# Performance work log

Hardware: AMD Instinct MI355X
Metric: run time of the kernel (lower is better)

Reference implementation:

```python
import jax, jax.numpy as jnp
from jax import lax
import numpy as np

RADIUS = 0.2
NSAMPLE = 64


def _ball_query(xyz, new_xyz, radius, nsample):
    """Faithful PointNet++ ball query.

    For each center, take the first `nsample` point indices (in index order)
    whose squared distance < radius^2; if fewer than nsample are found, the
    remaining slots are filled with the first found index (CUDA kernel
    semantics). Returns int32 idx of shape (B, npoint, nsample).
    """
    N = xyz.shape[1]
    # (B, npoint, N) squared distances
    d2 = jnp.sum((new_xyz[:, :, None, :] - xyz[:, None, :, :]) ** 2, axis=-1)
    within = d2 < (radius * radius)
    # key = point index if within ball, else N (sentinel); smallest nsample
    # keys == first nsample in-ball indices in index order.
    key = jnp.where(within, jnp.arange(N, dtype=jnp.int32), jnp.int32(N))
    neg_vals, _ = lax.top_k(-key, nsample)          # largest of -key = smallest key
    sel = -neg_vals                                  # (B, npoint, nsample)
    valid = sel < N
    first = jnp.where(valid[..., :1], sel[..., :1], 0)  # first found idx (or 0)
    return jnp.where(valid, sel, first)


def _group_gather(features, idx):
    # features: (B, C, N), idx: (B, npoint, nsample) -> (B, C, npoint, nsample)
    return jax.vmap(lambda f, i: f[:, i])(features, idx)


def setup_inputs() -> dict:
    key = jax.random.key(0)
    k1, k2, k3 = jax.random.split(key, 3)
    B, N, npoint, C = 4, 16384, 2048, 64
    xyz = jax.random.uniform(k1, (B, N, 3), dtype=jnp.float32)
    new_xyz = jax.random.uniform(k2, (B, npoint, 3), dtype=jnp.float32)
    features = jax.random.normal(k3, (B, C, N), dtype=jnp.float32)
    return {"xyz": xyz, "new_xyz": new_xyz, "features": features}


def reference(xyz, new_xyz, features):
    idx = _ball_query(xyz, new_xyz, RADIUS, NSAMPLE)          # (B, npoint, nsample)
    xyz_t = jnp.transpose(xyz, (0, 2, 1))                      # (B, 3, N)
    grouped_xyz = _group_gather(xyz_t, idx)                    # (B, 3, npoint, nsample)
    grouped_xyz = grouped_xyz - jnp.transpose(new_xyz, (0, 2, 1))[..., None]
    grouped_features = _group_gather(features, idx)            # (B, C, npoint, nsample)
    new_features = jnp.concatenate([grouped_xyz, grouped_features], axis=1)
    # original code does .transpose(1, 2) -> (B, npoint, 3+C, nsample)
    return jnp.transpose(new_features, (0, 2, 1, 3))
```

## Files before the change

### kernel.cpp

```cpp
#include <hip/hip_runtime.h>


#define BB 4
#define NN 16384
#define NP 2048
#define CC 64
#define NS 64
#define CH (3 + CC)
#define NCHUNK (NN / 256)

__global__ __launch_bounds__(256) void pn2_prep_kernel(
    const float* __restrict__ xyz,
    const float* __restrict__ new_xyz,
    const float* __restrict__ features,
    float* __restrict__ ft,
    int* __restrict__ idxbuf,
    float* __restrict__ out)
{
    __shared__ float tile[CC][65];
    __shared__ int sidx[4][NS];

    if (blockIdx.x < BB * 256) {
        const int b   = blockIdx.x >> 8;
        const int n0  = (blockIdx.x & 255) << 6;
        const int col = threadIdx.x & 63;
        const int r4  = threadIdx.x >> 6;
        const float* src = features + (size_t)b * CC * NN;
#pragma unroll
        for (int i = 0; i < 16; ++i) {
            const int c = r4 + i * 4;
            tile[c][col] = src[(size_t)c * NN + n0 + col];
        }
        __syncthreads();
        float* dst = ft + ((size_t)b * NN + n0) * CC;
#pragma unroll
        for (int i = 0; i < 16; ++i) {
            const int n = r4 + i * 4;
            dst[(size_t)n * CC + col] = tile[col][n];
        }
        return;
    }

    const int lane = threadIdx.x & 63;
    const int wave = threadIdx.x >> 6;
    const int center = (blockIdx.x - BB * 256) * 4 + wave;
    const int b = center >> 11;
    const int j = center & (NP - 1);

    const float r2 = 0.04f;
    const float* q = new_xyz + ((size_t)b * NP + j) * 3;
    const float cx = q[0], cy = q[1], cz = q[2];

    const float* xb = xyz + (size_t)b * NN * 3;
    const float4* x4 = (const float4*)xb;
    int* widx = sidx[wave];

    const int base = 3 * lane;
    int found = 0;
    int it = 0;
    float4 A = x4[base], Bv = x4[base + 1], Cv = x4[base + 2];

    while (true) {
        const int nit = (it + 1 < NCHUNK) ? it + 1 : it;
        const size_t nb = (size_t)nit * 192 + base;
        float4 nA = x4[nb], nB = x4[nb + 1], nC = x4[nb + 2];

        const int n0 = it * 256 + 4 * lane;
        const float px[4] = {A.x, A.w, Bv.z, Cv.y};
        const float py[4] = {A.y, Bv.x, Bv.w, Cv.z};
        const float pz[4] = {A.z, Bv.y, Cv.x, Cv.w};
        bool in[4];
        unsigned long long m[4];
#pragma unroll
        for (int k = 0; k < 4; ++k) {
            const float dx = px[k] - cx;
            const float dy = py[k] - cy;
            const float dz = pz[k] - cz;
            const float d2 = __fadd_rn(__fadd_rn(__fmul_rn(dx, dx), __fmul_rn(dy, dy)),
                                       __fmul_rn(dz, dz));
            in[k] = d2 < r2;
            m[k] = __ballot(in[k]);
        }
        const unsigned long long low = (1ull << lane) - 1ull;
        int pos = found
                + (int)__popcll(m[0] & low) + (int)__popcll(m[1] & low)
                + (int)__popcll(m[2] & low) + (int)__popcll(m[3] & low);
#pragma unroll
        for (int k = 0; k < 4; ++k) {
            if (in[k]) {
                if (pos < NS) widx[pos] = n0 + k;
                ++pos;
            }
        }
        found += (int)(__popcll(m[0]) + __popcll(m[1])
                     + __popcll(m[2]) + __popcll(m[3]));
        if (found >= NS || it == NCHUNK - 1) break;
        A = nA; Bv = nB; Cv = nC; ++it;
    }

    int myidx = 0;
    if (found > 0) {
        const int first = widx[0];
        myidx = (lane < found) ? widx[lane] : first;
    }
    idxbuf[(size_t)center * NS + lane] = myidx;

    const float* pp = xb + (size_t)myidx * 3;
    float* ob = out + ((size_t)center * CH) * NS + lane;
    __builtin_nontemporal_store(pp[0] - cx, ob + 0 * NS);
    __builtin_nontemporal_store(pp[1] - cy, ob + 1 * NS);
    __builtin_nontemporal_store(pp[2] - cz, ob + 2 * NS);
}

__global__ __launch_bounds__(256) void pn2_gather_kernel(
    const float* __restrict__ ft,
    const int* __restrict__ idxbuf,
    float* __restrict__ out)
{
    const int center = blockIdx.x;
    const int b = center >> 11;
    const int lane = threadIdx.x & 63;
    const int w = threadIdx.x >> 6;

    const int myidx = idxbuf[(size_t)center * NS + lane];
    const float4* row = (const float4*)(ft + ((size_t)b * NN + myidx) * CC) + 4 * w;
    const float4 v0 = row[0], v1 = row[1], v2 = row[2], v3 = row[3];

    float* ob = out + ((size_t)center * CH + 3 + 16 * w) * NS + lane;
    __builtin_nontemporal_store(v0.x, ob + 0 * NS);
    __builtin_nontemporal_store(v0.y, ob + 1 * NS);
    __builtin_nontemporal_store(v0.z, ob + 2 * NS);
    __builtin_nontemporal_store(v0.w, ob + 3 * NS);
    __builtin_nontemporal_store(v1.x, ob + 4 * NS);
    __builtin_nontemporal_store(v1.y, ob + 5 * NS);
    __builtin_nontemporal_store(v1.z, ob + 6 * NS);
    __builtin_nontemporal_store(v1.w, ob + 7 * NS);
    __builtin_nontemporal_store(v2.x, ob + 8 * NS);
    __builtin_nontemporal_store(v2.y, ob + 9 * NS);
    __builtin_nontemporal_store(v2.z, ob + 10 * NS);
    __builtin_nontemporal_store(v2.w, ob + 11 * NS);
    __builtin_nontemporal_store(v3.x, ob + 12 * NS);
    __builtin_nontemporal_store(v3.y, ob + 13 * NS);
    __builtin_nontemporal_store(v3.z, ob + 14 * NS);
    __builtin_nontemporal_store(v3.w, ob + 15 * NS);
}

__global__ __launch_bounds__(256, 4) void pn2_group_kernel(
    const float* __restrict__ xyz, const float* __restrict__ new_xyz,
    const float* __restrict__ features, float* __restrict__ out)
{
    __shared__ int sidx[4][NS];
    const int lane = threadIdx.x & 63;
    const int wave = threadIdx.x >> 6;
    const int center = blockIdx.x * 4 + wave;
    const int b = center >> 11;
    const int j = center & (NP - 1);
    const float r2 = 0.04f;
    const float* q = new_xyz + ((size_t)b * NP + j) * 3;
    const float cx = q[0], cy = q[1], cz = q[2];
    int* widx = sidx[wave];
    int found = 0;
    for (int it = 0; it < NN / 64; ++it) {
        const int n = it * 64 + lane;
        const float* p = xyz + ((size_t)b * NN + n) * 3;
        const float dx = p[0] - cx, dy = p[1] - cy, dz = p[2] - cz;
        const float d2 = __fadd_rn(__fadd_rn(__fmul_rn(dx, dx), __fmul_rn(dy, dy)),
                                   __fmul_rn(dz, dz));
        const bool within = d2 < r2;
        const unsigned long long mask = __ballot(within);
        const int pos = found + (int)__popcll(mask & ((1ull << lane) - 1ull));
        if (within && pos < NS) widx[pos] = n;
        found += (int)__popcll(mask);
        if (found >= NS) break;
    }
    int myidx = 0;
    if (found > 0) {
        const int first = widx[0];
        myidx = (lane < found) ? widx[lane] : first;
    }
    const float* pp = xyz + ((size_t)b * NN + myidx) * 3;
    float* ob = out + (((size_t)b * NP + j) * (size_t)CH) * NS + lane;
    ob[0 * NS] = pp[0] - cx;
    ob[1 * NS] = pp[1] - cy;
    ob[2 * NS] = pp[2] - cz;
    const float* fb = features + (size_t)b * CC * NN + myidx;
#pragma unroll 8
    for (int c = 0; c < CC; ++c) ob[(size_t)(3 + c) * NS] = fb[(size_t)c * NN];
}

extern "C" void kernel_launch(void* const* d_in, const int* in_sizes, int n_in,
                              void* d_out, int out_size, void* d_ws, size_t ws_size,
                              hipStream_t stream) {
    const float* xyz      = (const float*)d_in[0];
    const float* new_xyz  = (const float*)d_in[1];
    const float* features = (const float*)d_in[2];
    float* out = (float*)d_out;

    const size_t ft_bytes  = (size_t)BB * NN * CC * sizeof(float);
    const size_t idx_bytes = (size_t)BB * NP * NS * sizeof(int);

    if (ws_size >= ft_bytes + idx_bytes) {
        float* ft   = (float*)d_ws;
        int* idxbuf = (int*)((char*)d_ws + ft_bytes);
        pn2_prep_kernel<<<BB * 256 + BB * NP / 4, 256, 0, stream>>>(
            xyz, new_xyz, features, ft, idxbuf, out);
        pn2_gather_kernel<<<BB * NP, 256, 0, stream>>>(ft, idxbuf, out);
    } else {
        pn2_group_kernel<<<BB * NP / 4, 256, 0, stream>>>(xyz, new_xyz, features, out);
    }
}
```

Before: 54.52 us.

## Fuse ball query with feature gather, split transpose into its own kernel

The feature transpose moves into a separate kernel, and the ball query is fused with the feature gather, so each wave writes its center's whole output row directly. This drops the idx buffer round trip through global memory and one launch, but makes the transpose and query serial rather than co-scheduled in one grid. Each lane now loads a full 256-byte feature row (16 float4s in two batches of 8), which raises register pressure per wave. The transpose also switches to nontemporal loads.

```diff
diff --git a/kernel.cpp b/kernel.cpp
--- a/kernel.cpp
+++ b/kernel.cpp
@@ -9,41 +9,40 @@
 #define CH (3 + CC)
 #define NCHUNK (NN / 256)
 
-__global__ __launch_bounds__(256) void pn2_prep_kernel(
+__global__ __launch_bounds__(256) void pn2_transpose_kernel(
+    const float* __restrict__ f, float* __restrict__ ft)
+{
+    __shared__ float tile[CC][65];
+    const int b   = blockIdx.x >> 8;
+    const int n0  = (blockIdx.x & 255) << 6;
+    const int col = threadIdx.x & 63;
+    const int r4  = threadIdx.x >> 6;
+    const float* src = f + (size_t)b * CC * NN;
+#pragma unroll
+    for (int i = 0; i < 16; ++i) {
+        const int c = r4 + i * 4;
+        tile[c][col] = __builtin_nontemporal_load(&src[(size_t)c * NN + n0 + col]);
+    }
+    __syncthreads();
+    float* dst = ft + ((size_t)b * NN + n0) * CC;
+#pragma unroll
+    for (int i = 0; i < 16; ++i) {
+        const int n = r4 + i * 4;
+        dst[(size_t)n * CC + col] = tile[col][n];
+    }
+}
+
+__global__ __launch_bounds__(256, 4) void pn2_qg_kernel(
     const float* __restrict__ xyz,
     const float* __restrict__ new_xyz,
-    const float* __restrict__ features,
-    float* __restrict__ ft,
-    int* __restrict__ idxbuf,
+    const float* __restrict__ ft,
     float* __restrict__ out)
 {
-    __shared__ float tile[CC][65];
     __shared__ int sidx[4][NS];
-
-    if (blockIdx.x < BB * 256) {
-        const int b   = blockIdx.x >> 8;
-        const int n0  = (blockIdx.x & 255) << 6;
-        const int col = threadIdx.x & 63;
-        const int r4  = threadIdx.x >> 6;
-        const float* src = features + (size_t)b * CC * NN;
-#pragma unroll
-        for (int i = 0; i < 16; ++i) {
-            const int c = r4 + i * 4;
-            tile[c][col] = src[(size_t)c * NN + n0 + col];
-        }
-        __syncthreads();
-        float* dst = ft + ((size_t)b * NN + n0) * CC;
-#pragma unroll
-        for (int i = 0; i < 16; ++i) {
-            const int n = r4 + i * 4;
-            dst[(size_t)n * CC + col] = tile[col][n];
-        }
-        return;
-    }
 
     const int lane = threadIdx.x & 63;
     const int wave = threadIdx.x >> 6;
-    const int center = (blockIdx.x - BB * 256) * 4 + wave;
+    const int center = blockIdx.x * 4 + wave;
     const int b = center >> 11;
     const int j = center & (NP - 1);
 
@@ -56,6 +55,7 @@
     int* widx = sidx[wave];
 
     const int base = 3 * lane;
+    const unsigned long long low = (1ull << lane) - 1ull;
     int found = 0;
     int it = 0;
     float4 A = x4[base], Bv = x4[base + 1], Cv = x4[base + 2];
@@ -81,7 +81,6 @@
             in[k] = d2 < r2;
             m[k] = __ballot(in[k]);
         }
-        const unsigned long long low = (1ull << lane) - 1ull;
         int pos = found
                 + (int)__popcll(m[0] & low) + (int)__popcll(m[1] & low)
                 + (int)__popcll(m[2] & low) + (int)__popcll(m[3] & low);
@@ -103,46 +102,28 @@
         const int first = widx[0];
         myidx = (lane < found) ? widx[lane] : first;
     }
-    idxbuf[(size_t)center * NS + lane] = myidx;
 
     const float* pp = xb + (size_t)myidx * 3;
-    float* ob = out + ((size_t)center * CH) * NS + lane;
+    float* ob = out + (size_t)center * CH * NS + lane;
     __builtin_nontemporal_store(pp[0] - cx, ob + 0 * NS);
     __builtin_nontemporal_store(pp[1] - cy, ob + 1 * NS);
     __builtin_nontemporal_store(pp[2] - cz, ob + 2 * NS);
-}
 
-__global__ __launch_bounds__(256) void pn2_gather_kernel(
-    const float* __restrict__ ft,
-    const int* __restrict__ idxbuf,
-    float* __restrict__ out)
-{
-    const int center = blockIdx.x;
-    const int b = center >> 11;
-    const int lane = threadIdx.x & 63;
-    const int w = threadIdx.x >> 6;
-
-    const int myidx = idxbuf[(size_t)center * NS + lane];
-    const float4* row = (const float4*)(ft + ((size_t)b * NN + myidx) * CC) + 4 * w;
-    const float4 v0 = row[0], v1 = row[1], v2 = row[2], v3 = row[3];
-
-    float* ob = out + ((size_t)center * CH + 3 + 16 * w) * NS + lane;
-    __builtin_nontemporal_store(v0.x, ob + 0 * NS);
-    __builtin_nontemporal_store(v0.y, ob + 1 * NS);
-    __builtin_nontemporal_store(v0.z, ob + 2 * NS);
-    __builtin_nontemporal_store(v0.w, ob + 3 * NS);
-    __builtin_nontemporal_store(v1.x, ob + 4 * NS);
-    __builtin_nontemporal_store(v1.y, ob + 5 * NS);
-    __builtin_nontemporal_store(v1.z, ob + 6 * NS);
-    __builtin_nontemporal_store(v1.w, ob + 7 * NS);
-    __builtin_nontemporal_store(v2.x, ob + 8 * NS);
-    __builtin_nontemporal_store(v2.y, ob + 9 * NS);
-    __builtin_nontemporal_store(v2.z, ob + 10 * NS);
-    __builtin_nontemporal_store(v2.w, ob + 11 * NS);
-    __builtin_nontemporal_store(v3.x, ob + 12 * NS);
-    __builtin_nontemporal_store(v3.y, ob + 13 * NS);
-    __builtin_nontemporal_store(v3.z, ob + 14 * NS);
-    __builtin_nontemporal_store(v3.w, ob + 15 * NS);
+    const float4* frow = (const float4*)(ft + ((size_t)b * NN + myidx) * CC);
+#pragma unroll
+    for (int p = 0; p < 2; ++p) {
+        float4 v[8];
+#pragma unroll
+        for (int i = 0; i < 8; ++i) v[i] = frow[8 * p + i];
+        float* o2 = ob + (size_t)(3 + 32 * p) * NS;
+#pragma unroll
+        for (int i = 0; i < 8; ++i) {
+            __builtin_nontemporal_store(v[i].x, o2 + (size_t)(4 * i + 0) * NS);
+            __builtin_nontemporal_store(v[i].y, o2 + (size_t)(4 * i + 1) * NS);
+            __builtin_nontemporal_store(v[i].z, o2 + (size_t)(4 * i + 2) * NS);
+            __builtin_nontemporal_store(v[i].w, o2 + (size_t)(4 * i + 3) * NS);
+        }
+    }
 }
 
 __global__ __launch_bounds__(256, 4) void pn2_group_kernel(
@@ -196,15 +177,12 @@
     const float* features = (const float*)d_in[2];
     float* out = (float*)d_out;
 
-    const size_t ft_bytes  = (size_t)BB * NN * CC * sizeof(float);
-    const size_t idx_bytes = (size_t)BB * NP * NS * sizeof(int);
+    const size_t ft_bytes = (size_t)BB * NN * CC * sizeof(float);
 
-    if (ws_size >= ft_bytes + idx_bytes) {
-        float* ft   = (float*)d_ws;
-        int* idxbuf = (int*)((char*)d_ws + ft_bytes);
-        pn2_prep_kernel<<<BB * 256 + BB * NP / 4, 256, 0, stream>>>(
-            xyz, new_xyz, features, ft, idxbuf, out);
-        pn2_gather_kernel<<<BB * NP, 256, 0, stream>>>(ft, idxbuf, out);
+    if (ws_size >= ft_bytes) {
+        float* ft = (float*)d_ws;
+        pn2_transpose_kernel<<<BB * 256, 256, 0, stream>>>(features, ft);
+        pn2_qg_kernel<<<BB * NP / 4, 256, 0, stream>>>(xyz, new_xyz, ft, out);
     } else {
         pn2_group_kernel<<<BB * NP / 4, 256, 0, stream>>>(xyz, new_xyz, features, out);
     }
```

Measured after the change: 54.43 us. About the same (-0.2%).
